# Kernel tuning notes

Measured on AMD Instinct MI355X. Metric: run time of the kernel, lower is better.

## Reference

```python
import jax, jax.numpy as jnp
import numpy as np

B, P, D, N, K = 8, 784, 1536, 20000, 9


def setup_inputs() -> dict:
    key = jax.random.key(0)
    k1, k2 = jax.random.split(key)
    x = jax.random.normal(k1, (B, P, D), dtype=jnp.float32)       # patch embeddings [B, P, D]
    memory = jax.random.normal(k2, (N, D), dtype=jnp.float32)     # FAISS memory bank [N, D]
    return {"x": x, "memory": memory, "k": K}


def reference(x, memory, k):
    # Squared L2 distances (FAISS IndexFlatL2 convention): [B, P, N]
    x2 = jnp.sum(x * x, axis=-1, keepdims=True)                   # [B, P, 1]
    m2 = jnp.sum(memory * memory, axis=-1)                        # [N]
    d = x2 + m2[None, None, :] - 2.0 * jnp.einsum('bpd,nd->bpn', x, memory)
    # k nearest (smallest distances, ascending) -> score_patches [B, P, k]
    neg_topk, _ = jax.lax.top_k(-d, k)
    score_patches = -neg_topk
    closest_dist = score_patches[..., 0]                          # [B, P]
    idxmax = jnp.argmax(closest_dist, axis=1)                     # [B]
    # N_b: the k neighbor distances of the worst (max closest-dist) patch
    N_b = jnp.take_along_axis(score_patches, idxmax[:, None, None], axis=1)[:, 0, :]  # [B, k]
    N_b = N_b - jnp.max(N_b, axis=1, keepdims=True)               # numerical stabilization (as in source)
    N_b_exp = jnp.exp(N_b)
    w = 1.0 - jnp.max(N_b_exp, axis=1) / jnp.sum(N_b_exp, axis=1)  # [B]
    score = w * jnp.max(closest_dist, axis=1)                      # [B]
    return score
```

## Files before the change

kernel.cpp:

```cpp
#include <hip/hip_runtime.h>
#include <math.h>

#define B_    8
#define P_    784
#define M_    6272
#define D_    1536
#define N_    20000
#define NC_   8

#define MPAD  6400
#define NPAD2 20224
#define MT2   25
#define NT2   79
#define KT2   12

#define NBLK  1250

using i32x8  = __attribute__((ext_vector_type(8))) int;
using f32x4v = __attribute__((ext_vector_type(4))) float;

#define GLD_LDS16(src, dst)                                            \
  __builtin_amdgcn_global_load_lds(                                    \
      (__attribute__((address_space(1))) const void*)(src),            \
      (__attribute__((address_space(3))) void*)(dst), 16, 0, 0)

__device__ __forceinline__ unsigned fenc(float f) {
  unsigned u = __float_as_uint(f);
  return (u >> 31) ? ~u : (u | 0x80000000u);
}
__device__ __forceinline__ float fdec(unsigned k) {
  return (k >> 31) ? __uint_as_float(k & 0x7FFFFFFFu) : __uint_as_float(~k);
}

__device__ __forceinline__ void ins9(float* t, float v) {
  float tim1 = t[0];
  t[0] = fminf(t[0], v);
#pragma unroll
  for (int i = 1; i < 9; ++i) {
    float cur = t[i];
    t[i] = fminf(cur, fmaxf(tim1, v));
    tim1 = cur;
  }
}

__device__ __forceinline__ void convert_one(const float* __restrict__ src,
                                            unsigned char* __restrict__ dst,
                                            float* __restrict__ sq,
                                            int row, int realrows) {
  const int t = threadIdx.x;
  if (row >= realrows) {
    unsigned* w = (unsigned*)(dst + (size_t)row * D_);
    for (int i = t; i < D_ / 4; i += 256) w[i] = 0u;
    if (t == 0) sq[row] = 1e30f;
    return;
  }
  const float4* r4 = (const float4*)(src + (size_t)row * D_);
  unsigned* w = (unsigned*)(dst + (size_t)row * D_);
  float s = 0.f;
  for (int i = t; i < D_ / 4; i += 256) {
    float4 v = r4[i];
    s += v.x * v.x + v.y * v.y + v.z * v.z + v.w * v.w;
    int pk = __builtin_amdgcn_cvt_pk_fp8_f32(v.x, v.y, 0, false);
    pk     = __builtin_amdgcn_cvt_pk_fp8_f32(v.z, v.w, pk, true);
    w[i] = (unsigned)pk;
  }
#pragma unroll
  for (int m = 32; m >= 1; m >>= 1) s += __shfl_xor(s, m);
  __shared__ float ws4[4];
  if ((t & 63) == 0) ws4[t >> 6] = s;
  __syncthreads();
  if (t == 0) sq[row] = ws4[0] + ws4[1] + ws4[2] + ws4[3];
}

__global__ void convert_all(const float* __restrict__ x, const float* __restrict__ mem,
                            unsigned char* __restrict__ xq, unsigned char* __restrict__ mq,
                            float* __restrict__ x2, float* __restrict__ m2,
                            unsigned* __restrict__ closest_enc) {
  const int blk = blockIdx.x;
  if (blk < MPAD / 256)
    closest_enc[blk * 256 + threadIdx.x] = 0xFFFFFFFFu;
  if (blk < NPAD2) convert_one(mem, mq, m2, blk, N_);
  else convert_one(x, xq, x2, blk - NPAD2, M_);
}

__global__ __launch_bounds__(512, 2) void gemm_min8(
    const unsigned char* __restrict__ xq, const unsigned char* __restrict__ mq,
    const float* __restrict__ m2, unsigned* __restrict__ closest_enc) {
  __shared__ __attribute__((aligned(16))) char ldsFlat[131072];
  __shared__ float ldsMin[4][256];

  const int NWG = MT2 * NT2;
  const int bid = blockIdx.x;
  const int q = NWG >> 3, r = NWG & 7;
  const int xcd = bid & 7, loc = bid >> 3;
  const int wg = (xcd < r ? xcd * (q + 1) : r * (q + 1) + (xcd - r) * q) + loc;
  const int s = wg / (5 * NT2);
  const int r2 = wg - s * (5 * NT2);
  const int mT = s * 5 + (r2 % 5);
  const int nT = r2 / 5;

  const int tid = threadIdx.x;
  const int lane = tid & 63, wid = tid >> 6;
  const int wm = wid >> 2, wn = wid & 3;
  const int g = lane >> 4, r16 = lane & 15;
  const int mBase = mT * 256, nBase = nT * 256;

  const int stRow = wid * 8 + (lane >> 3);
  const int stA = mBase + stRow;
  const int stB = nBase + stRow;
  const int cswz16 = ((lane & 7) ^ ((lane >> 3) & 7)) * 16;

  const int csl = (g * 32) ^ ((r16 & 7) << 4);
  const int csh = csl ^ 16;
  const int rdA = wm * 16384 + r16 * 128;
  const int rdB = wn * 8192 + r16 * 128;

#define STAGE(matsel, srcp, rowb, bufb, h, ktv) do {                        \
    char* dst_ = ldsFlat + (matsel) * 65536 + (bufb) * 32768 +              \
                 (h) * 16384 + wid * 1024;                                  \
    const unsigned char* s_ =                                               \
        (srcp) + (size_t)((rowb) + (h) * 128) * 1536 + (ktv) * 128 + cswz16;\
    GLD_LDS16(s_, dst_);                                                    \
    GLD_LDS16(s_ + 64 * 1536, dst_ + 8192);                                 \
  } while (0)

#define LDFRAG(base, off) ({                                                \
    int4 lo_ = *(const int4*)((base) + (off) + csl);                        \
    int4 hi_ = *(const int4*)((base) + (off) + csh);                        \
    i32x8{lo_.x, lo_.y, lo_.z, lo_.w, hi_.x, hi_.y, hi_.z, hi_.w}; })

#define MFMA8(a, b, c) __builtin_amdgcn_mfma_scale_f32_16x16x128_f8f6f4(    \
    (a), (b), (c), 0, 0, 0, 0x7F7F7F7F, 0, 0x7F7F7F7F)

  f32x4v acc[8][4];
#pragma unroll
  for (int i = 0; i < 8; ++i)
#pragma unroll
    for (int j = 0; j < 4; ++j) acc[i][j] = f32x4v{0.f, 0.f, 0.f, 0.f};

  STAGE(1, mq, stB, 0, 0, 0);
  STAGE(1, mq, stB, 0, 1, 0);
  STAGE(0, xq, stA, 0, 0, 0);
  STAGE(0, xq, stA, 0, 1, 0);
  STAGE(1, mq, stB, 1, 0, 1);
  STAGE(1, mq, stB, 1, 1, 1);
  asm volatile("s_waitcnt vmcnt(4)");
  __builtin_amdgcn_s_barrier();
  __builtin_amdgcn_sched_barrier(0);

#pragma unroll 1
  for (int kt = 0; kt < KT2; ++kt) {
    const int bufc = kt & 1;
    const char* Ab = ldsFlat + bufc * 32768;
    const char* Bb = ldsFlat + 65536 + bufc * 32768;
    const bool stgA = (kt + 1) < KT2;
    const bool stgB = (kt + 2) < KT2;
    i32x8 bf[4], af[4];

#pragma unroll
    for (int nf = 0; nf < 4; ++nf) bf[nf] = LDFRAG(Bb, rdB + nf * 2048);
#pragma unroll
    for (int mf = 0; mf < 4; ++mf) af[mf] = LDFRAG(Ab, rdA + mf * 2048);
    if (stgA) {
      STAGE(0, xq, stA, bufc ^ 1, 0, kt + 1);
      STAGE(0, xq, stA, bufc ^ 1, 1, kt + 1);
    }
    __builtin_amdgcn_s_barrier();
    asm volatile("s_waitcnt lgkmcnt(0)");
    __builtin_amdgcn_s_setprio(1);
#pragma unroll
    for (int mf = 0; mf < 4; ++mf)
#pragma unroll
      for (int nf = 0; nf < 4; ++nf)
        acc[mf][nf] = MFMA8(af[mf], bf[nf], acc[mf][nf]);
    __builtin_amdgcn_s_setprio(0);
    __builtin_amdgcn_s_barrier();

#pragma unroll
    for (int mf = 0; mf < 4; ++mf) af[mf] = LDFRAG(Ab, rdA + (mf + 4) * 2048);
    if (stgB) {
      STAGE(1, mq, stB, bufc, 0, kt + 2);
      STAGE(1, mq, stB, bufc, 1, kt + 2);
    }
    __builtin_amdgcn_s_barrier();
    asm volatile("s_waitcnt lgkmcnt(0)");
    __builtin_amdgcn_s_setprio(1);
#pragma unroll
    for (int mf = 0; mf < 4; ++mf)
#pragma unroll
      for (int nf = 0; nf < 4; ++nf)
        acc[mf + 4][nf] = MFMA8(af[mf], bf[nf], acc[mf + 4][nf]);
    __builtin_amdgcn_s_setprio(0);
    if (kt >= KT2 - 2) {
      asm volatile("s_waitcnt vmcnt(0)");
    } else {
      asm volatile("s_waitcnt vmcnt(4)");
    }
    __builtin_amdgcn_s_barrier();
    __builtin_amdgcn_sched_barrier(0);
  }
#undef STAGE
#undef LDFRAG
#undef MFMA8

  float m2v[4];
#pragma unroll
  for (int nf = 0; nf < 4; ++nf) m2v[nf] = m2[nBase + wn * 64 + nf * 16 + r16];
#pragma unroll
  for (int mf = 0; mf < 8; ++mf) {
    float mn[4];
#pragma unroll
    for (int i = 0; i < 4; ++i) {
      float v = m2v[0] - 2.f * acc[mf][0][i];
      v = fminf(v, m2v[1] - 2.f * acc[mf][1][i]);
      v = fminf(v, m2v[2] - 2.f * acc[mf][2][i]);
      v = fminf(v, m2v[3] - 2.f * acc[mf][3][i]);
      mn[i] = v;
    }
#pragma unroll
    for (int msk = 1; msk < 16; msk <<= 1)
#pragma unroll
      for (int i = 0; i < 4; ++i) mn[i] = fminf(mn[i], __shfl_xor(mn[i], msk));
    if (r16 == 0)
#pragma unroll
      for (int i = 0; i < 4; ++i)
        ldsMin[wn][wm * 128 + mf * 16 + g * 4 + i] = mn[i];
  }
  __syncthreads();
  if (tid < 256) {
    float v = fminf(fminf(ldsMin[0][tid], ldsMin[1][tid]),
                    fminf(ldsMin[2][tid], ldsMin[3][tid]));
    atomicMin(&closest_enc[mBase + tid], fenc(v));
  }
}

__global__ void topcand_kernel(const unsigned* __restrict__ closest_enc,
                               const float* __restrict__ x2,
                               int* __restrict__ cand) {
  const int b = blockIdx.x;
  const int t = threadIdx.x;
  __shared__ float cls[P_];
  for (int p = t; p < P_; p += 256) {
    const int row = b * P_ + p;
    cls[p] = x2[row] + fdec(closest_enc[row]);
  }
  __syncthreads();
  __shared__ float wv[4];
  __shared__ int wi_[4];
  __shared__ int picked[NC_];
  for (int r = 0; r < NC_; ++r) {
    float mv = -3e38f; int mi = 1 << 30;
    for (int p = t; p < P_; p += 256) {
      bool skip = false;
      for (int c = 0; c < r; ++c) skip |= (picked[c] == p);
      float v = cls[p];
      if (!skip && (v > mv || (v == mv && p < mi))) { mv = v; mi = p; }
    }
#pragma unroll
    for (int m = 32; m >= 1; m >>= 1) {
      float ov = __shfl_xor(mv, m); int oi = __shfl_xor(mi, m);
      if (ov > mv || (ov == mv && oi < mi)) { mv = ov; mi = oi; }
    }
    if ((t & 63) == 0) { wv[t >> 6] = mv; wi_[t >> 6] = mi; }
    __syncthreads();
    if (t == 0) {
      float bv = wv[0]; int bi = wi_[0];
      for (int w = 1; w < 4; ++w)
        if (wv[w] > bv || (wv[w] == bv && wi_[w] < bi)) { bv = wv[w]; bi = wi_[w]; }
      picked[r] = bi;
      cand[b * NC_ + r] = bi;
    }
    __syncthreads();
  }
}

__global__ __launch_bounds__(256) void cand_dist9(
    const float* __restrict__ x, const float* __restrict__ mem,
    const float* __restrict__ x2, const float* __restrict__ m2,
    const int* __restrict__ cand, float* __restrict__ ctop) {
  const int wid = threadIdx.x >> 6, lane = threadIdx.x & 63;
  const int blk = blockIdx.x;
  __shared__ float ldsD[B_ * NC_][20];

  const int rbase = blk * 16 + wid * 4;
  float4 m4[4][6];
  float m2r[4];
#pragma unroll
  for (int k = 0; k < 4; ++k) {
    const float4* mrow = (const float4*)(mem + (size_t)(rbase + k) * D_);
#pragma unroll
    for (int j = 0; j < 6; ++j) m4[k][j] = mrow[j * 64 + lane];
    m2r[k] = m2[rbase + k];
  }
#pragma unroll 2
  for (int bc = 0; bc < B_ * NC_; ++bc) {
    const int b = bc / NC_;
    const int p = cand[bc];
    const float4* xp = (const float4*)(x + ((size_t)b * P_ + p) * D_);
    float s0 = 0.f, s1 = 0.f, s2 = 0.f, s3 = 0.f;
#pragma unroll
    for (int j = 0; j < 6; ++j) {
      float4 a = xp[j * 64 + lane];
      s0 += a.x * m4[0][j].x + a.y * m4[0][j].y + a.z * m4[0][j].z + a.w * m4[0][j].w;
      s1 += a.x * m4[1][j].x + a.y * m4[1][j].y + a.z * m4[1][j].z + a.w * m4[1][j].w;
      s2 += a.x * m4[2][j].x + a.y * m4[2][j].y + a.z * m4[2][j].z + a.w * m4[2][j].w;
      s3 += a.x * m4[3][j].x + a.y * m4[3][j].y + a.z * m4[3][j].z + a.w * m4[3][j].w;
    }
#pragma unroll
    for (int msk = 32; msk >= 1; msk >>= 1) {
      s0 += __shfl_xor(s0, msk); s1 += __shfl_xor(s1, msk);
      s2 += __shfl_xor(s2, msk); s3 += __shfl_xor(s3, msk);
    }
    if (lane == 0) {
      const float xx = x2[b * P_ + p];
      ldsD[bc][wid * 4 + 0] = xx + m2r[0] - 2.f * s0;
      ldsD[bc][wid * 4 + 1] = xx + m2r[1] - 2.f * s1;
      ldsD[bc][wid * 4 + 2] = xx + m2r[2] - 2.f * s2;
      ldsD[bc][wid * 4 + 3] = xx + m2r[3] - 2.f * s3;
    }
  }
  __syncthreads();
  if (lane < 16) {
    const int bc = wid * 16 + lane;
    float t[9];
#pragma unroll
    for (int i = 0; i < 9; ++i) t[i] = 3e38f;
#pragma unroll
    for (int i = 0; i < 16; ++i) ins9(t, ldsD[bc][i]);
    float* o = ctop + ((size_t)bc * NBLK + blk) * 9;
#pragma unroll
    for (int i = 0; i < 9; ++i) o[i] = t[i];
  }
}

__global__ void merge_top9(const float* __restrict__ ctop, float* __restrict__ top9) {
  const int bc = blockIdx.x;
  const float* d = ctop + (size_t)bc * (NBLK * 9);
  float t[9];
#pragma unroll
  for (int i = 0; i < 9; ++i) t[i] = 3e38f;
  for (int n = threadIdx.x; n < NBLK * 9; n += 256) ins9(t, d[n]);
  __shared__ float l9[256 * 9];
  __shared__ float l9b[32 * 9];
#pragma unroll
  for (int i = 0; i < 9; ++i) l9[threadIdx.x * 9 + i] = t[i];
  __syncthreads();
  if (threadIdx.x < 32) {
    float u[9];
#pragma unroll
    for (int i = 0; i < 9; ++i) u[i] = 3e38f;
    for (int s = 0; s < 8; ++s)
#pragma unroll
      for (int i = 0; i < 9; ++i) ins9(u, l9[(threadIdx.x * 8 + s) * 9 + i]);
#pragma unroll
    for (int i = 0; i < 9; ++i) l9b[threadIdx.x * 9 + i] = u[i];
  }
  __syncthreads();
  if (threadIdx.x == 0) {
    float u[9];
#pragma unroll
    for (int i = 0; i < 9; ++i) u[i] = 3e38f;
    for (int s = 0; s < 32; ++s)
#pragma unroll
      for (int i = 0; i < 9; ++i) ins9(u, l9b[s * 9 + i]);
#pragma unroll
    for (int i = 0; i < 9; ++i) top9[bc * 9 + i] = u[i];
  }
}

__global__ void score_kernel(const float* __restrict__ top9, const int* __restrict__ cand,
                             float* __restrict__ out) {
  const int b = threadIdx.x;
  if (b >= B_) return;
  float bestv = -3e38f; int bestc = 0, bestp = 1 << 30;
  for (int c = 0; c < NC_; ++c) {
    float v = top9[(b * NC_ + c) * 9 + 0];
    int p = cand[b * NC_ + c];
    if (v > bestv || (v == bestv && p < bestp)) { bestv = v; bestc = c; bestp = p; }
  }
  const float* v9 = &top9[(b * NC_ + bestc) * 9];
  float mx = v9[8];
  float sum = 0.f, mxe = 0.f;
  for (int i = 0; i < 9; ++i) {
    float e = expf(v9[i] - mx);
    sum += e;
    if (e > mxe) mxe = e;
  }
  out[b] = (1.f - mxe / sum) * bestv;
}

extern "C" void kernel_launch(void* const* d_in, const int* in_sizes, int n_in,
                              void* d_out, int out_size, void* d_ws, size_t ws_size,
                              hipStream_t stream) {
  const float* x = (const float*)d_in[0];
  const float* mem = (const float*)d_in[1];
  float* out = (float*)d_out;
  char* ws = (char*)d_ws;

  unsigned char* xq    = (unsigned char*)(ws);
  unsigned char* mq    = (unsigned char*)(ws + 9830400);
  float* x2            = (float*)(ws + 40894464);
  float* m2            = (float*)(ws + 40920064);
  unsigned* closest_enc= (unsigned*)(ws + 41000960);
  int*   cand          = (int*)  (ws + 41026560);
  float* ctop          = (float*)(ws + 41026816);
  float* top9          = (float*)(ws + 43906816);

  convert_all<<<NPAD2 + MPAD, 256, 0, stream>>>(x, mem, xq, mq, x2, m2, closest_enc);
  gemm_min8<<<MT2 * NT2, 512, 0, stream>>>(xq, mq, m2, closest_enc);
  topcand_kernel<<<B_, 256, 0, stream>>>(closest_enc, x2, cand);
  cand_dist9<<<NBLK, 256, 0, stream>>>(x, mem, x2, m2, cand, ctop);
  merge_top9<<<B_ * NC_, 256, 0, stream>>>(ctop, top9);
  score_kernel<<<1, 64, 0, stream>>>(top9, cand, out);
}
```

Baseline: 443.1 us.

## Load B fragments directly from global into registers, stage only A in LDS

The memory-bank operand B now skips LDS staging and is loaded straight from global memory into register fragments, double-buffered across k-steps. Only the x operand is staged through LDS, which halves LDS use and removes B's LDS reads and some barriers. The loop is unrolled by two so the two register buffers swap roles, and it now waits on vmcnt(0) every step. In exchange, each wave makes uncoalesced global reads of B fragments, the register count goes up, and wave groups no longer share B through LDS, so global/L2 traffic for B rises.

```diff
diff --git a/kernel.cpp b/kernel.cpp
--- a/kernel.cpp
+++ b/kernel.cpp
@@ -86,7 +86,7 @@
 __global__ __launch_bounds__(512, 2) void gemm_min8(
     const unsigned char* __restrict__ xq, const unsigned char* __restrict__ mq,
     const float* __restrict__ m2, unsigned* __restrict__ closest_enc) {
-  __shared__ __attribute__((aligned(16))) char ldsFlat[131072];
+  __shared__ __attribute__((aligned(16))) char ldsA[65536];
   __shared__ float ldsMin[4][256];
 
   const int NWG = MT2 * NT2;
@@ -105,23 +105,31 @@
   const int g = lane >> 4, r16 = lane & 15;
   const int mBase = mT * 256, nBase = nT * 256;
 
-  const int stRow = wid * 8 + (lane >> 3);
-  const int stA = mBase + stRow;
-  const int stB = nBase + stRow;
+  const int stA = mBase + wid * 8 + (lane >> 3);
   const int cswz16 = ((lane & 7) ^ ((lane >> 3) & 7)) * 16;
 
   const int csl = (g * 32) ^ ((r16 & 7) << 4);
   const int csh = csl ^ 16;
   const int rdA = wm * 16384 + r16 * 128;
-  const int rdB = wn * 8192 + r16 * 128;
-
-#define STAGE(matsel, srcp, rowb, bufb, h, ktv) do {                        \
-    char* dst_ = ldsFlat + (matsel) * 65536 + (bufb) * 32768 +              \
-                 (h) * 16384 + wid * 1024;                                  \
+
+  const unsigned char* bbase = mq + (size_t)(nBase + wn * 64 + r16) * 1536 + g * 32;
+
+#define STAGEA(bufb, h, ktv) do {                                           \
+    char* dst_ = ldsA + (bufb) * 32768 + (h) * 16384 + wid * 1024;          \
     const unsigned char* s_ =                                               \
-        (srcp) + (size_t)((rowb) + (h) * 128) * 1536 + (ktv) * 128 + cswz16;\
+        xq + (size_t)((stA) + (h) * 128) * 1536 + (ktv) * 128 + cswz16;     \
     GLD_LDS16(s_, dst_);                                                    \
     GLD_LDS16(s_ + 64 * 1536, dst_ + 8192);                                 \
+  } while (0)
+
+#define LOADB(dst, ktv) do {                                                \
+    _Pragma("unroll")                                                       \
+    for (int nf_ = 0; nf_ < 4; ++nf_) {                                     \
+      const unsigned char* bp_ = bbase + (size_t)nf_ * 16 * 1536 + (ktv) * 128; \
+      int4 lo_ = *(const int4*)bp_;                                         \
+      int4 hi_ = *(const int4*)(bp_ + 16);                                  \
+      dst[nf_] = i32x8{lo_.x, lo_.y, lo_.z, lo_.w, hi_.x, hi_.y, hi_.z, hi_.w}; \
+    }                                                                       \
   } while (0)
 
 #define LDFRAG(base, off) ({                                                \
@@ -138,68 +146,56 @@
 #pragma unroll
     for (int j = 0; j < 4; ++j) acc[i][j] = f32x4v{0.f, 0.f, 0.f, 0.f};
 
-  STAGE(1, mq, stB, 0, 0, 0);
-  STAGE(1, mq, stB, 0, 1, 0);
-  STAGE(0, xq, stA, 0, 0, 0);
-  STAGE(0, xq, stA, 0, 1, 0);
-  STAGE(1, mq, stB, 1, 0, 1);
-  STAGE(1, mq, stB, 1, 1, 1);
-  asm volatile("s_waitcnt vmcnt(4)");
+  i32x8 bf0[4], bf1[4];
+
+  STAGEA(0, 0, 0);
+  STAGEA(0, 1, 0);
+  LOADB(bf0, 0);
+  asm volatile("s_waitcnt vmcnt(0)");
   __builtin_amdgcn_s_barrier();
   __builtin_amdgcn_sched_barrier(0);
 
+#define KTBODY(ktv, BFC, BFN) do {                                          \
+    const char* Ab_ = ldsA + ((ktv) & 1) * 32768;                           \
+    i32x8 af_[4];                                                           \
+    _Pragma("unroll")                                                       \
+    for (int mf_ = 0; mf_ < 4; ++mf_) af_[mf_] = LDFRAG(Ab_, rdA + mf_ * 2048); \
+    if ((ktv) + 1 < KT2) {                                                  \
+      STAGEA(((ktv) & 1) ^ 1, 0, (ktv) + 1);                                \
+      STAGEA(((ktv) & 1) ^ 1, 1, (ktv) + 1);                                \
+      LOADB(BFN, (ktv) + 1);                                                \
+    }                                                                       \
+    asm volatile("s_waitcnt lgkmcnt(0)");                                   \
+    __builtin_amdgcn_s_setprio(1);                                          \
+    _Pragma("unroll")                                                       \
+    for (int mf_ = 0; mf_ < 4; ++mf_)                                       \
+      _Pragma("unroll")                                                     \
+      for (int nf_ = 0; nf_ < 4; ++nf_)                                     \
+        acc[mf_][nf_] = MFMA8(af_[mf_], BFC[nf_], acc[mf_][nf_]);           \
+    __builtin_amdgcn_s_setprio(0);                                          \
+    _Pragma("unroll")                                                       \
+    for (int mf_ = 0; mf_ < 4; ++mf_) af_[mf_] = LDFRAG(Ab_, rdA + (mf_ + 4) * 2048); \
+    asm volatile("s_waitcnt lgkmcnt(0)");                                   \
+    __builtin_amdgcn_s_setprio(1);                                          \
+    _Pragma("unroll")                                                       \
+    for (int mf_ = 0; mf_ < 4; ++mf_)                                       \
+      _Pragma("unroll")                                                     \
+      for (int nf_ = 0; nf_ < 4; ++nf_)                                     \
+        acc[mf_ + 4][nf_] = MFMA8(af_[mf_], BFC[nf_], acc[mf_ + 4][nf_]);   \
+    __builtin_amdgcn_s_setprio(0);                                          \
+    asm volatile("s_waitcnt vmcnt(0)");                                     \
+    __builtin_amdgcn_s_barrier();                                           \
+    __builtin_amdgcn_sched_barrier(0);                                      \
+  } while (0)
+
 #pragma unroll 1
-  for (int kt = 0; kt < KT2; ++kt) {
-    const int bufc = kt & 1;
-    const char* Ab = ldsFlat + bufc * 32768;
-    const char* Bb = ldsFlat + 65536 + bufc * 32768;
-    const bool stgA = (kt + 1) < KT2;
-    const bool stgB = (kt + 2) < KT2;
-    i32x8 bf[4], af[4];
-
-#pragma unroll
-    for (int nf = 0; nf < 4; ++nf) bf[nf] = LDFRAG(Bb, rdB + nf * 2048);
-#pragma unroll
-    for (int mf = 0; mf < 4; ++mf) af[mf] = LDFRAG(Ab, rdA + mf * 2048);
-    if (stgA) {
-      STAGE(0, xq, stA, bufc ^ 1, 0, kt + 1);
-      STAGE(0, xq, stA, bufc ^ 1, 1, kt + 1);
-    }
-    __builtin_amdgcn_s_barrier();
-    asm volatile("s_waitcnt lgkmcnt(0)");
-    __builtin_amdgcn_s_setprio(1);
-#pragma unroll
-    for (int mf = 0; mf < 4; ++mf)
-#pragma unroll
-      for (int nf = 0; nf < 4; ++nf)
-        acc[mf][nf] = MFMA8(af[mf], bf[nf], acc[mf][nf]);
-    __builtin_amdgcn_s_setprio(0);
-    __builtin_amdgcn_s_barrier();
-
-#pragma unroll
-    for (int mf = 0; mf < 4; ++mf) af[mf] = LDFRAG(Ab, rdA + (mf + 4) * 2048);
-    if (stgB) {
-      STAGE(1, mq, stB, bufc, 0, kt + 2);
-      STAGE(1, mq, stB, bufc, 1, kt + 2);
-    }
-    __builtin_amdgcn_s_barrier();
-    asm volatile("s_waitcnt lgkmcnt(0)");
-    __builtin_amdgcn_s_setprio(1);
-#pragma unroll
-    for (int mf = 0; mf < 4; ++mf)
-#pragma unroll
-      for (int nf = 0; nf < 4; ++nf)
-        acc[mf + 4][nf] = MFMA8(af[mf], bf[nf], acc[mf + 4][nf]);
-    __builtin_amdgcn_s_setprio(0);
-    if (kt >= KT2 - 2) {
-      asm volatile("s_waitcnt vmcnt(0)");
-    } else {
-      asm volatile("s_waitcnt vmcnt(4)");
-    }
-    __builtin_amdgcn_s_barrier();
-    __builtin_amdgcn_sched_barrier(0);
-  }
-#undef STAGE
+  for (int ktp = 0; ktp < KT2 / 2; ++ktp) {
+    KTBODY(2 * ktp,     bf0, bf1);
+    KTBODY(2 * ktp + 1, bf1, bf0);
+  }
+#undef KTBODY
+#undef STAGEA
+#undef LOADB
 #undef LDFRAG
 #undef MFMA8
 
```

New measurement: 1.197 ms. +170.2%, slower.
